# Kernel optimization log

Hardware: AMD Instinct MI355X
Metric: run time of the kernel (lower is better)

The kernel has to match this reference:

```python
import jax, jax.numpy as jnp
import numpy as np

N, E, D, C, L, G = 50000, 1600000, 128, 10, 4, 512
BN_EPS = 1e-5


def setup_inputs() -> dict:
    key = jax.random.key(0)
    ks = jax.random.split(key, 16)
    s = 0.05  # weight init scale
    inp = {
        "x": jax.random.normal(ks[0], (N, D), dtype=jnp.float32),
        "edge_index": jax.random.randint(ks[1], (2, E), 0, N, dtype=jnp.int32),
        "batch": jnp.sort(jax.random.randint(ks[2], (N,), 0, G, dtype=jnp.int32)),
        "num_graphs": G,
        # GINConv inner MLP params (layer 0 input dim == D since num_features == num_hidden)
        "conv_W1": jax.random.normal(ks[3], (L, D, D), dtype=jnp.float32) * s,
        "conv_b1": jnp.zeros((L, D), dtype=jnp.float32),
        "conv_bn_g": jnp.ones((L, D), dtype=jnp.float32),
        "conv_bn_b": jnp.zeros((L, D), dtype=jnp.float32),
        "conv_W2": jax.random.normal(ks[4], (L, D, D), dtype=jnp.float32) * s,
        "conv_b2": jnp.zeros((L, D), dtype=jnp.float32),
        # outer BatchNorm after each conv
        "bn_g": jnp.ones((L, D), dtype=jnp.float32),
        "bn_b": jnp.zeros((L, D), dtype=jnp.float32),
        # per-scale classifier heads (L+1 of them; fcs[0] input dim == num_features == D)
        "fc_W": jax.random.normal(ks[5], (L + 1, D, C), dtype=jnp.float32) * s,
        "fc_b": jnp.zeros((L + 1, C), dtype=jnp.float32),
    }
    return inp


def _bn(h, g, b):
    # BatchNorm1d in training mode: batch stats over nodes, biased variance
    m = h.mean(axis=0)
    v = jnp.mean((h - m) ** 2, axis=0)
    return (h - m) * jax.lax.rsqrt(v + BN_EPS) * g + b


def reference(x, edge_index, batch, num_graphs, conv_W1, conv_b1, conv_bn_g,
              conv_bn_b, conv_W2, conv_b2, bn_g, bn_b, fc_W, fc_b):
    n_nodes = x.shape[0]
    src, dst = edge_index[0], edge_index[1]
    outs = [x]
    h = x
    for i in range(L):
        # GINConv (eps=0, aggr='add'): mlp(x + scatter_add of neighbor features)
        agg = jax.ops.segment_sum(h[src], dst, num_segments=n_nodes)  # [N, D]
        z = h + agg
        z = z @ conv_W1[i] + conv_b1[i]
        z = jax.nn.relu(_bn(z, conv_bn_g[i], conv_bn_b[i]))
        z = z @ conv_W2[i] + conv_b2[i]
        h = jax.nn.relu(_bn(z, bn_g[i], bn_b[i]))
        outs.append(h)
    out = None
    for i, o in enumerate(outs):
        pooled = jax.ops.segment_sum(o, batch, num_segments=num_graphs)  # [G, D]
        logits = pooled @ fc_W[i] + fc_b[i]
        out = logits if out is None else out + logits
    return jax.nn.log_softmax(out, axis=-1)
```

## Files before the change

### kernel.cpp

```cpp
#include <hip/hip_runtime.h>

#define NN 50000
#define EE 1600000
#define DD 128
#define CC 10
#define LLAY 4
#define GG 512
#define GD (GG*DD)
#define NB 196
#define BK_EDGES 1600
#define BUCKCAP 16000
#define NSUB 16
#define SUBW 3125
#define WPAD 136

static constexpr float BN_EPS = 1e-5f;
static constexpr float INV_N = 1.0f / (float)NN;

typedef __bf16 bf16x8 __attribute__((ext_vector_type(8)));
typedef float f32x4 __attribute__((ext_vector_type(4)));

static __device__ __forceinline__ float bflo(unsigned u){ return __uint_as_float(u << 16); }
static __device__ __forceinline__ float bfhi(unsigned u){ return __uint_as_float(u & 0xffff0000u); }
static __device__ __forceinline__ unsigned short f2bf(float f){
    unsigned u = __float_as_uint(f);
    return (unsigned short)((u + 0x7fffu + ((u >> 16) & 1u)) >> 16);
}
static __device__ __forceinline__ unsigned packbf(float a, float b){
    return (unsigned)f2bf(a) | ((unsigned)f2bf(b) << 16);
}
static __device__ __forceinline__ bf16x8 ldfrag(const unsigned short* p){
    union { uint4 u; bf16x8 b; } t; t.u = *(const uint4*)p; return t.b;
}
static __device__ __forceinline__ bf16x8 asfrag(uint4 u){
    union { uint4 u; bf16x8 b; } t; t.u = u; return t.b;
}


__global__ void zero_k(int* p, int n){
    int i = blockIdx.x * 256 + threadIdx.x;
    if (i < n) p[i] = 0;
}

__global__ void wprep_k(const float* __restrict__ W1, const float* __restrict__ W2,
                        unsigned short* __restrict__ Wtall){
    int idx = blockIdx.x * 256 + threadIdx.x;
    int mat = idx >> 14; int rr = idx & 16383;
    int k = rr >> 7; int j = rr & 127;
    const float* Wsrc = (mat < 4) ? (W1 + mat * 16384) : (W2 + (mat - 4) * 16384);
    Wtall[mat * 16384 + j * 128 + k] = f2bf(Wsrc[k * 128 + j]);
}

__global__ void gsearch_k(const int* __restrict__ batch, int* __restrict__ gstart){
    int g = blockIdx.x * 256 + threadIdx.x;
    if (g <= GG){
        int lo = 0, hi = NN;
        while (lo < hi){ int mid = (lo + hi) >> 1; if (batch[mid] < g) lo = mid + 1; else hi = mid; }
        gstart[g] = lo;
    }
}

__global__ __launch_bounds__(256) void binA_k(const int* __restrict__ srcA,
                                              const int* __restrict__ dstA,
                                              int* __restrict__ bucketCur,
                                              unsigned* __restrict__ binned){
    __shared__ int cnt[NB], bas[NB], off[NB];
    int tid = threadIdx.x;
    if (tid < NB){ cnt[tid] = 0; off[tid] = 0; }
    __syncthreads();
    int e0 = blockIdx.x * BK_EDGES;
    for (int i = tid; i < BK_EDGES; i += 256){
        int e = e0 + i;
        if (e < EE) atomicAdd(&cnt[dstA[e] >> 8], 1);
    }
    __syncthreads();
    if (tid < NB && cnt[tid] > 0) bas[tid] = atomicAdd(&bucketCur[tid], cnt[tid]);
    __syncthreads();
    for (int i = tid; i < BK_EDGES; i += 256){
        int e = e0 + i;
        if (e < EE){
            int d = dstA[e]; int b = d >> 8;
            int p = b * BUCKCAP + bas[b] + atomicAdd(&off[b], 1);
            binned[p] = (unsigned)srcA[e] | ((unsigned)(d & 255) << 17);
        }
    }
}

__global__ __launch_bounds__(256) void bscan_k(const int* __restrict__ bucketCur,
                                               int* __restrict__ bucketBase,
                                               int* __restrict__ rp){
    __shared__ int lds[256];
    int t = threadIdx.x;
    int v = (t < NB) ? bucketCur[t] : 0;
    lds[t] = v; __syncthreads();
    for (int o = 1; o < 256; o <<= 1){
        int xv = 0; if (t >= o) xv = lds[t - o];
        __syncthreads(); lds[t] += xv; __syncthreads();
    }
    int excl = lds[t] - v;
    if (t < NB) bucketBase[t] = excl;
    if (t == 0){ bucketBase[NB] = EE; rp[NN] = EE; }
}

__global__ __launch_bounds__(1024) void binB_k(const unsigned* __restrict__ binned,
                                               const int* __restrict__ bucketCur,
                                               const int* __restrict__ bucketBase,
                                               int* __restrict__ rp,
                                               int* __restrict__ ssort){
    __shared__ int c16[256 * NSUB];
    __shared__ int b16[256 * NSUB];
    __shared__ int nt[256];
    int b = blockIdx.x, tid = threadIdx.x;
    int nb0 = b * 256;
    int nmax = NN - nb0; if (nmax > 256) nmax = 256;
    for (int i = tid; i < 256 * NSUB; i += 1024) c16[i] = 0;
    __syncthreads();
    int cntb = bucketCur[b];
    int src0 = b * BUCKCAP;
    int base = bucketBase[b];
    for (int i = tid; i < cntb; i += 1024){
        unsigned u = binned[src0 + i];
        int src = (int)(u & 0x1FFFFu); int dl = (int)(u >> 17);
        atomicAdd(&c16[dl * NSUB + src / SUBW], 1);
    }
    __syncthreads();
    int cc[NSUB]; int tot = 0;
    if (tid < 256){
        #pragma unroll
        for (int k = 0; k < NSUB; k++){ cc[k] = c16[tid * NSUB + k]; tot += cc[k]; }
        nt[tid] = tot;
    }
    __syncthreads();
    for (int o = 1; o < 256; o <<= 1){
        int xv = 0;
        if (tid < 256 && tid >= o) xv = nt[tid - o];
        __syncthreads();
        if (tid < 256) nt[tid] += xv;
        __syncthreads();
    }
    if (tid < 256){
        int p = base + nt[tid] - tot;
        if (tid < nmax) rp[nb0 + tid] = p;
        int run = p;
        #pragma unroll
        for (int k = 0; k < NSUB; k++){ b16[tid * NSUB + k] = run; run += cc[k]; }
    }
    __syncthreads();
    for (int i = tid; i < 256 * NSUB; i += 1024) c16[i] = 0;
    __syncthreads();
    for (int i = tid; i < cntb; i += 1024){
        unsigned u = binned[src0 + i];
        int src = (int)(u & 0x1FFFFu); int dl = (int)(u >> 17);
        int t = src / SUBW;
        int pos = b16[dl * NSUB + t] + atomicAdd(&c16[dl * NSUB + t], 1);
        ssort[pos] = src;
    }
}

__global__ __launch_bounds__(256) void convxpool_k(const float2* __restrict__ x2,
                                                   const int* __restrict__ gstart,
                                                   unsigned* __restrict__ h32,
                                                   float* __restrict__ outp){
    __shared__ float sd[512];
    int b = blockIdx.x; int gid = b >> 2, chunk = b & 3;
    int tid = threadIdx.x; int c = tid & 63, rs = tid >> 6;
    int s = gstart[gid], e = gstart[gid + 1];
    float a0 = 0.f, a1 = 0.f;
    for (int n = s + chunk * 4 + rs; n < e; n += 16){
        float2 v = x2[n * 64 + c];
        h32[n * 64 + c] = packbf(v.x, v.y);
        a0 += v.x; a1 += v.y;
    }
    sd[tid] = a0; sd[256 + tid] = a1; __syncthreads();
    if (tid < 64){
        float r0 = 0.f, r1 = 0.f;
        #pragma unroll
        for (int k2 = 0; k2 < 4; k2++){ r0 += sd[tid + 64 * k2]; r1 += sd[256 + tid + 64 * k2]; }
        atomicAdd(&outp[gid * 128 + 2 * tid], r0);
        atomicAdd(&outp[gid * 128 + 2 * tid + 1], r1);
    }
}


__global__ __launch_bounds__(256) void agg_k(const unsigned* __restrict__ h32,
                                             const int* __restrict__ rp,
                                             const int* __restrict__ ssort,
                                             unsigned* __restrict__ z32,
                                             float* __restrict__ zstats){
    int tid = threadIdx.x;
    if (blockIdx.x == 0) zstats[tid] = 0.f;
    int n = blockIdx.x * 4 + (tid >> 6);
    int lane = tid & 63;
    unsigned self = h32[n * 64 + lane];
    float ax = bflo(self), ay = bfhi(self);
    int e  = __builtin_amdgcn_readfirstlane(rp[n]);
    int e1 = __builtin_amdgcn_readfirstlane(rp[n + 1]);
    for (; e + 15 < e1; e += 16){
        int sA[16];
        #pragma unroll
        for (int k = 0; k < 16; k++) sA[k] = ssort[e + k];
        unsigned uA[16];
        #pragma unroll
        for (int k = 0; k < 16; k++) uA[k] = h32[sA[k] * 64 + lane];
        #pragma unroll
        for (int k = 0; k < 16; k++){ ax += bflo(uA[k]); ay += bfhi(uA[k]); }
    }
    for (; e + 3 < e1; e += 4){
        int s0 = ssort[e], s1 = ssort[e + 1], s2 = ssort[e + 2], s3 = ssort[e + 3];
        unsigned u0 = h32[s0 * 64 + lane];
        unsigned u1 = h32[s1 * 64 + lane];
        unsigned u2 = h32[s2 * 64 + lane];
        unsigned u3 = h32[s3 * 64 + lane];
        ax += bflo(u0) + bflo(u1); ay += bfhi(u0) + bfhi(u1);
        ax += bflo(u2) + bflo(u3); ay += bfhi(u2) + bfhi(u3);
    }
    for (; e < e1; ++e){
        unsigned u0 = h32[ssort[e] * 64 + lane];
        ax += bflo(u0); ay += bfhi(u0);
    }
    z32[n * 64 + lane] = packbf(ax, ay);
}

template<int TR>
__global__ __launch_bounds__(256) void gemm_k(const unsigned* __restrict__ A32,
                                              const unsigned short* __restrict__ Wtg,
                                              const float* __restrict__ bias,
                                              unsigned short* __restrict__ Cst,
                                              const float* __restrict__ stats,
                                              const float* __restrict__ gma,
                                              const float* __restrict__ bta,
                                              float* __restrict__ ostats,
                                              float* __restrict__ zstats,
                                              float* __restrict__ zpool){
    __shared__ __align__(16) unsigned short Wl[64 * WPAD];
    __shared__ float sred[512];
    __shared__ __align__(16) float sl[128], tl[128];
    int tid = threadIdx.x;
    int slice = blockIdx.x & 1;
    int tileb = blockIdx.x >> 1;

    int wv = tid >> 6, lane = tid & 63;
    int rowbase = tileb * 128 + wv * 32;
    int r0 = rowbase + (lane & 15);
    int r1 = r0 + 16;
    int kd = (lane >> 4) * 4;
    uint4 va[4], vb[4];
    #pragma unroll
    for (int ks = 0; ks < 4; ks++){
        va[ks] = (r0 < NN) ? *(const uint4*)(A32 + r0 * 64 + ks * 16 + kd) : make_uint4(0,0,0,0);
        vb[ks] = (r1 < NN) ? *(const uint4*)(A32 + r1 * 64 + ks * 16 + kd) : make_uint4(0,0,0,0);
    }

    if (blockIdx.x == 0 && zstats) zstats[tid] = 0.f;
    if (zpool && blockIdx.x < 256) zpool[blockIdx.x * 256 + tid] = 0.f;
    {
        const uint4* src = (const uint4*)(Wtg + slice * 64 * 128);
        uint4* dst = (uint4*)Wl;
        #pragma unroll
        for (int i = 0; i < 4; i++){
            int idx = tid + 256 * i;
            int row = idx >> 4, c16 = idx & 15;
            dst[row * (WPAD / 8) + c16] = src[idx];
        }
    }
    if (TR && tid < 128){
        float mean = stats[tid] * INV_N;
        float q    = stats[128 + tid] * INV_N;
        float inv  = rsqrtf(q - mean * mean + BN_EPS);
        float s    = gma[tid] * inv;
        sl[tid] = s; tl[tid] = bta[tid] - mean * s;
    }
    __syncthreads();

    if (TR){
        #pragma unroll
        for (int ks = 0; ks < 4; ks++){
            int q = ks * 8 + (lane >> 4) * 2;
            float4 sA = ((const float4*)sl)[q], sB = ((const float4*)sl)[q + 1];
            float4 tA = ((const float4*)tl)[q], tB = ((const float4*)tl)[q + 1];
            float fs[8] = {sA.x, sA.y, sA.z, sA.w, sB.x, sB.y, sB.z, sB.w};
            float ft[8] = {tA.x, tA.y, tA.z, tA.w, tB.x, tB.y, tB.z, tB.w};
            unsigned* pa = (unsigned*)&va[ks];
            unsigned* pb = (unsigned*)&vb[ks];
            #pragma unroll
            for (int c = 0; c < 4; c++){
                float f0 = fmaxf(bflo(pa[c]) * fs[2*c] + ft[2*c], 0.f);
                float f1 = fmaxf(bfhi(pa[c]) * fs[2*c+1] + ft[2*c+1], 0.f);
                pa[c] = packbf(f0, f1);
                f0 = fmaxf(bflo(pb[c]) * fs[2*c] + ft[2*c], 0.f);
                f1 = fmaxf(bfhi(pb[c]) * fs[2*c+1] + ft[2*c+1], 0.f);
                pb[c] = packbf(f0, f1);
            }
        }
    }

    f32x4 acc[2][4];
    #pragma unroll
    for (int a = 0; a < 2; a++)
        #pragma unroll
        for (int b = 0; b < 4; b++) acc[a][b] = (f32x4){0.f, 0.f, 0.f, 0.f};

    #pragma unroll
    for (int ks = 0; ks < 4; ks++){
        int wk = ks * 32 + (lane >> 4) * 8;
        bf16x8 a0 = asfrag(va[ks]);
        bf16x8 a1 = asfrag(vb[ks]);
        #pragma unroll
        for (int ct = 0; ct < 4; ++ct){
            bf16x8 b = ldfrag(&Wl[(ct * 16 + (lane & 15)) * WPAD + wk]);
            acc[0][ct] = __builtin_amdgcn_mfma_f32_16x16x32_bf16(a0, b, acc[0][ct], 0, 0, 0);
            acc[1][ct] = __builtin_amdgcn_mfma_f32_16x16x32_bf16(a1, b, acc[1][ct], 0, 0, 0);
        }
    }

    int cl = lane & 15, rq = lane >> 4;
    float colS[4], colQ[4];
    #pragma unroll
    for (int ct = 0; ct < 4; ++ct){
        int col = slice * 64 + ct * 16 + cl;
        float bv = bias[col];
        float ps = 0.f, pq = 0.f;
        #pragma unroll
        for (int rt = 0; rt < 2; ++rt){
            #pragma unroll
            for (int rr2 = 0; rr2 < 4; ++rr2){
                int grow = rowbase + rt * 16 + rq * 4 + rr2;
                if (grow < NN){
                    float val = acc[rt][ct][rr2] + bv;
                    Cst[grow * 128 + col] = f2bf(val);
                    ps += val; pq += val * val;
                }
            }
        }
        ps += __shfl_xor(ps, 16); pq += __shfl_xor(pq, 16);
        ps += __shfl_xor(ps, 32); pq += __shfl_xor(pq, 32);
        colS[ct] = ps; colQ[ct] = pq;
    }
    if (rq == 0){
        #pragma unroll
        for (int ct = 0; ct < 4; ++ct){
            sred[wv * 64 + ct * 16 + cl]       = colS[ct];
            sred[256 + wv * 64 + ct * 16 + cl] = colQ[ct];
        }
    }
    __syncthreads();
    if (tid < 64){
        float s1 = sred[tid] + sred[64 + tid] + sred[128 + tid] + sred[192 + tid];
        float s2 = sred[256 + tid] + sred[320 + tid] + sred[384 + tid] + sred[448 + tid];
        atomicAdd(&ostats[slice * 64 + tid], s1);
        atomicAdd(&ostats[128 + slice * 64 + tid], s2);
    }
}

__global__ __launch_bounds__(256) void ewpool_k(const unsigned* __restrict__ z32,
                                                const float* __restrict__ stats,
                                                const float* __restrict__ g,
                                                const float* __restrict__ b,
                                                const int* __restrict__ gstart,
                                                unsigned* __restrict__ h32,
                                                float* __restrict__ outp){
    __shared__ float sd[512];
    int blk = blockIdx.x; int gid = blk >> 2, chunk = blk & 3;
    int tid = threadIdx.x;
    int c = tid & 63, rs = tid >> 6;
    int c2 = c * 2;
    float m0 = stats[c2] * INV_N,     q0 = stats[128 + c2] * INV_N;
    float inv0 = rsqrtf(q0 - m0 * m0 + BN_EPS);
    float s0 = g[c2] * inv0, t0 = b[c2] - m0 * s0;
    float m1 = stats[c2 + 1] * INV_N, q1 = stats[129 + c2] * INV_N;
    float inv1 = rsqrtf(q1 - m1 * m1 + BN_EPS);
    float s1 = g[c2 + 1] * inv1, t1 = b[c2 + 1] - m1 * s1;
    int s = gstart[gid], e = gstart[gid + 1];
    float a0 = 0.f, a1 = 0.f;
    int n = s + chunk * 4 + rs;
    for (; n + 16 < e; n += 32){
        unsigned u0 = z32[n * 64 + c];
        unsigned u1 = z32[(n + 16) * 64 + c];
        float f0, f1;
        f0 = fmaxf(bflo(u0) * s0 + t0, 0.f); f1 = fmaxf(bfhi(u0) * s1 + t1, 0.f);
        h32[n * 64 + c] = packbf(f0, f1); a0 += f0; a1 += f1;
        f0 = fmaxf(bflo(u1) * s0 + t0, 0.f); f1 = fmaxf(bfhi(u1) * s1 + t1, 0.f);
        h32[(n + 16) * 64 + c] = packbf(f0, f1); a0 += f0; a1 += f1;
    }
    for (; n < e; n += 16){
        unsigned u = z32[n * 64 + c];
        float f0 = fmaxf(bflo(u) * s0 + t0, 0.f);
        float f1 = fmaxf(bfhi(u) * s1 + t1, 0.f);
        h32[n * 64 + c] = packbf(f0, f1);
        a0 += f0; a1 += f1;
    }
    sd[tid] = a0; sd[256 + tid] = a1; __syncthreads();
    if (tid < 64){
        float r0 = 0.f, r1 = 0.f;
        #pragma unroll
        for (int k2 = 0; k2 < 4; k2++){ r0 += sd[tid + 64 * k2]; r1 += sd[256 + tid + 64 * k2]; }
        atomicAdd(&outp[gid * 128 + 2 * tid], r0);
        atomicAdd(&outp[gid * 128 + 2 * tid + 1], r1);
    }
}

__global__ __launch_bounds__(64) void final_k(const float* __restrict__ pooled,
                                              const float* __restrict__ fcW,
                                              const float* __restrict__ fcb,
                                              float* __restrict__ out){
    int g = blockIdx.x, l = threadIdx.x;
    float p0[5], p1[5];
    #pragma unroll
    for (int i = 0; i < 5; i++){
        p0[i] = pooled[i * GD + g * 128 + l];
        p1[i] = pooled[i * GD + g * 128 + 64 + l];
    }
    float lg[10];
    #pragma unroll
    for (int c2 = 0; c2 < 10; c2++){
        float s = 0;
        #pragma unroll
        for (int i = 0; i < 5; i++){
            s += p0[i] * fcW[(i * 128 + l) * 10 + c2];
            s += p1[i] * fcW[(i * 128 + 64 + l) * 10 + c2];
        }
        #pragma unroll
        for (int off = 32; off >= 1; off >>= 1) s += __shfl_down(s, off);
        lg[c2] = s;
    }
    if (l == 0){
        #pragma unroll
        for (int c2 = 0; c2 < 10; c2++){
            float bs = 0;
            #pragma unroll
            for (int i = 0; i < 5; i++) bs += fcb[i * 10 + c2];
            lg[c2] += bs;
        }
        float mx = lg[0];
        #pragma unroll
        for (int c2 = 1; c2 < 10; c2++) mx = fmaxf(mx, lg[c2]);
        float se = 0;
        #pragma unroll
        for (int c2 = 0; c2 < 10; c2++) se += expf(lg[c2] - mx);
        float lse = mx + logf(se);
        #pragma unroll
        for (int c2 = 0; c2 < 10; c2++) out[g * 10 + c2] = lg[c2] - lse;
    }
}


extern "C" void kernel_launch(void* const* d_in, const int* in_sizes, int n_in,
                              void* d_out, int out_size, void* d_ws, size_t ws_size,
                              hipStream_t stream){
    (void)in_sizes; (void)n_in; (void)out_size; (void)ws_size;
    const float* x     = (const float*)d_in[0];
    const int*   ei    = (const int*)d_in[1];
    const int*   batch = (const int*)d_in[2];
    const float* cW1   = (const float*)d_in[4];
    const float* cb1   = (const float*)d_in[5];
    const float* cbng  = (const float*)d_in[6];
    const float* cbnb  = (const float*)d_in[7];
    const float* cW2   = (const float*)d_in[8];
    const float* cb2   = (const float*)d_in[9];
    const float* bng   = (const float*)d_in[10];
    const float* bnb   = (const float*)d_in[11];
    const float* fcW   = (const float*)d_in[12];
    const float* fcb   = (const float*)d_in[13];

    char* base = (char*)d_ws;
    size_t off = 0;
    auto alloc = [&](size_t bytes) -> void* {
        void* p = base + off;
        off = (off + bytes + 255) & ~(size_t)255;
        return p;
    };
    unsigned*       hB     = (unsigned*)alloc((size_t)NN * 64 * 4);
    unsigned*       zA     = (unsigned*)alloc((size_t)NN * 64 * 4);
    unsigned*       zB     = (unsigned*)alloc((size_t)NN * 64 * 4);
    unsigned short* Wtall  = (unsigned short*)alloc(8 * 16384 * 2);
    int*            ssort  = (int*)alloc((size_t)EE * 4);
    int*            rp     = (int*)alloc((NN + 1) * 4);
    int*            gstart = (int*)alloc((GG + 1) * 4);
    int*            bucketBase = (int*)alloc((NB + 1) * 4);
    int*            bucketCur  = (int*)alloc(NB * 4);
    float*          pooled = (float*)alloc((size_t)5 * GD * 4);
    float*          stats1 = (float*)alloc(256 * 4);
    float*          stats2 = (float*)alloc(256 * 4);
    unsigned*       binned = (unsigned*)zB;

    int zwords = (int)(((char*)(pooled + GD) - (char*)bucketCur) / 4);

    zero_k<<<(zwords + 255) / 256, 256, 0, stream>>>(bucketCur, zwords);
    wprep_k<<<512, 256, 0, stream>>>(cW1, cW2, Wtall);
    gsearch_k<<<3, 256, 0, stream>>>(batch, gstart);
    binA_k<<<(EE + BK_EDGES - 1) / BK_EDGES, 256, 0, stream>>>(ei, ei + EE, bucketCur, binned);
    bscan_k<<<1, 256, 0, stream>>>(bucketCur, bucketBase, rp);
    binB_k<<<NB, 1024, 0, stream>>>(binned, bucketCur, bucketBase, rp, ssort);
    convxpool_k<<<4 * GG, 256, 0, stream>>>((const float2*)x, gstart, hB, pooled);

    const int gemmGrid = 2 * ((NN + 127) / 128);
    for (int i = 0; i < LLAY; i++){
        agg_k<<<NN / 4, 256, 0, stream>>>(hB, rp, ssort, zA, stats1);
        gemm_k<0><<<gemmGrid, 256, 0, stream>>>(zA, Wtall + i * 16384, cb1 + i * 128,
                                                (unsigned short*)zB,
                                                nullptr, nullptr, nullptr, stats1, stats2, nullptr);
        gemm_k<1><<<gemmGrid, 256, 0, stream>>>(zB, Wtall + (4 + i) * 16384, cb2 + i * 128,
                                                (unsigned short*)zA,
                                                stats1, cbng + i * 128, cbnb + i * 128, stats2, nullptr,
                                                pooled + (size_t)(i + 1) * GD);
        ewpool_k<<<4 * GG, 256, 0, stream>>>(zA, stats2, bng + i * 128, bnb + i * 128,
                                             gstart, hB, pooled + (size_t)(i + 1) * GD);
    }
    final_k<<<GG, 64, 0, stream>>>(pooled, fcW, fcb, (float*)d_out);
}
```

Before: 544.7 us.

## Quantize node features to 8-bit for neighbor aggregation gather

Adds per-column max tracking: a max-abs pass over x, and running min/max of the second GEMM output fed through the BN affine. With these, features are stored as 8-bit codes alongside bf16. The aggregation kernel now gathers 1-byte-per-feature rows and sums them with packed integer adds in 16-bit lanes, splitting the wave into two halves that take alternate edge groups. It then dequantizes once per node using the scale and offset times degree. This cuts gather traffic in the memory-bound aggregation, at the cost of 8-bit quantization error in the summed neighbor features, extra kernels and atomics, and a risk of packed-lane overflow at high degree (safe only for degree up to about 257).

```diff
diff --git a/kernel.cpp b/kernel.cpp
--- a/kernel.cpp
+++ b/kernel.cpp
@@ -29,6 +29,14 @@
 static __device__ __forceinline__ unsigned packbf(float a, float b){
     return (unsigned)f2bf(a) | ((unsigned)f2bf(b) << 16);
 }
+static __device__ __forceinline__ unsigned encf(float f){
+    unsigned b = __float_as_uint(f);
+    return (b & 0x80000000u) ? ~b : (b | 0x80000000u);
+}
+static __device__ __forceinline__ float decf(unsigned e){
+    unsigned b = (e & 0x80000000u) ? (e ^ 0x80000000u) : ~e;
+    return __uint_as_float(b);
+}
 static __device__ __forceinline__ bf16x8 ldfrag(const unsigned short* p){
     union { uint4 u; bf16x8 b; } t; t.u = *(const uint4*)p; return t.b;
 }
@@ -157,18 +165,47 @@
     }
 }
 
+__global__ __launch_bounds__(256) void xmax_k(const float* __restrict__ x,
+                                              unsigned* __restrict__ xmaxE){
+    __shared__ float sm[256];
+    int tid = threadIdx.x;
+    int col = tid & 127, rh = tid >> 7;
+    float m = 0.f;
+    for (int r = blockIdx.x * 2 + rh; r < NN; r += 1024)
+        m = fmaxf(m, fabsf(x[r * 128 + col]));
+    sm[tid] = m; __syncthreads();
+    if (tid < 128){
+        m = fmaxf(sm[tid], sm[tid + 128]);
+        atomicMax(&xmaxE[col], __float_as_uint(m));
+    }
+}
+
+__global__ void qx_k(const unsigned* __restrict__ xmaxE,
+                     float* __restrict__ qD, float* __restrict__ qR){
+    int c = threadIdx.x;
+    float m = __uint_as_float(xmaxE[c]);
+    qD[c] = m * (1.f / 127.f);
+    qR[c] = (m > 0.f) ? 127.f / m : 0.f;
+}
+
 __global__ __launch_bounds__(256) void convxpool_k(const float2* __restrict__ x2,
                                                    const int* __restrict__ gstart,
                                                    unsigned* __restrict__ h32,
+                                                   unsigned short* __restrict__ h8u,
+                                                   const float* __restrict__ qR0,
                                                    float* __restrict__ outp){
     __shared__ float sd[512];
     int b = blockIdx.x; int gid = b >> 2, chunk = b & 3;
     int tid = threadIdx.x; int c = tid & 63, rs = tid >> 6;
     int s = gstart[gid], e = gstart[gid + 1];
+    float2 rv = ((const float2*)qR0)[c];
     float a0 = 0.f, a1 = 0.f;
     for (int n = s + chunk * 4 + rs; n < e; n += 16){
         float2 v = x2[n * 64 + c];
         h32[n * 64 + c] = packbf(v.x, v.y);
+        int i0 = (int)rintf(v.x * rv.x) + 128; i0 = min(max(i0, 0), 255);
+        int i1 = (int)rintf(v.y * rv.y) + 128; i1 = min(max(i1, 0), 255);
+        h8u[n * 64 + c] = (unsigned short)(i0 | (i1 << 8));
         a0 += v.x; a1 += v.y;
     }
     sd[tid] = a0; sd[256 + tid] = a1; __syncthreads();
@@ -183,42 +220,66 @@
 
 
 __global__ __launch_bounds__(256) void agg_k(const unsigned* __restrict__ h32,
+                                             const unsigned char* __restrict__ h8,
                                              const int* __restrict__ rp,
                                              const int* __restrict__ ssort,
+                                             const float* __restrict__ qD,
+                                             float offv,
                                              unsigned* __restrict__ z32,
                                              float* __restrict__ zstats){
     int tid = threadIdx.x;
     if (blockIdx.x == 0) zstats[tid] = 0.f;
     int n = blockIdx.x * 4 + (tid >> 6);
     int lane = tid & 63;
-    unsigned self = h32[n * 64 + lane];
-    float ax = bflo(self), ay = bfhi(self);
+    int grp = lane >> 5;
+    int d   = lane & 31;
+    const unsigned* hq = (const unsigned*)h8;
+    const unsigned M = 0x00FF00FFu;
     int e  = __builtin_amdgcn_readfirstlane(rp[n]);
     int e1 = __builtin_amdgcn_readfirstlane(rp[n + 1]);
-    for (; e + 15 < e1; e += 16){
+    int deg = e1 - e;
+    unsigned accE = 0, accO = 0;
+    for (; e + 31 < e1; e += 32){
         int sA[16];
         #pragma unroll
-        for (int k = 0; k < 16; k++) sA[k] = ssort[e + k];
+        for (int k = 0; k < 16; k++) sA[k] = ssort[e + grp * 16 + k];
         unsigned uA[16];
         #pragma unroll
-        for (int k = 0; k < 16; k++) uA[k] = h32[sA[k] * 64 + lane];
-        #pragma unroll
-        for (int k = 0; k < 16; k++){ ax += bflo(uA[k]); ay += bfhi(uA[k]); }
-    }
-    for (; e + 3 < e1; e += 4){
-        int s0 = ssort[e], s1 = ssort[e + 1], s2 = ssort[e + 2], s3 = ssort[e + 3];
-        unsigned u0 = h32[s0 * 64 + lane];
-        unsigned u1 = h32[s1 * 64 + lane];
-        unsigned u2 = h32[s2 * 64 + lane];
-        unsigned u3 = h32[s3 * 64 + lane];
-        ax += bflo(u0) + bflo(u1); ay += bfhi(u0) + bfhi(u1);
-        ax += bflo(u2) + bflo(u3); ay += bfhi(u2) + bfhi(u3);
-    }
-    for (; e < e1; ++e){
-        unsigned u0 = h32[ssort[e] * 64 + lane];
-        ax += bflo(u0); ay += bfhi(u0);
-    }
-    z32[n * 64 + lane] = packbf(ax, ay);
+        for (int k = 0; k < 16; k++) uA[k] = hq[sA[k] * 32 + d];
+        #pragma unroll
+        for (int k = 0; k < 16; k++){ accE += uA[k] & M; accO += (uA[k] >> 8) & M; }
+    }
+    for (; e + 7 < e1; e += 8){
+        int sA[4];
+        #pragma unroll
+        for (int k = 0; k < 4; k++) sA[k] = ssort[e + grp * 4 + k];
+        #pragma unroll
+        for (int k = 0; k < 4; k++){
+            unsigned u = hq[sA[k] * 32 + d];
+            accE += u & M; accO += (u >> 8) & M;
+        }
+    }
+    for (; e + 1 < e1; e += 2){
+        unsigned u = hq[ssort[e + grp] * 32 + d];
+        accE += u & M; accO += (u >> 8) & M;
+    }
+    if (e < e1 && grp == 0){
+        unsigned u = hq[ssort[e] * 32 + d];
+        accE += u & M; accO += (u >> 8) & M;
+    }
+    accE += __shfl_xor(accE, 32);
+    accO += __shfl_xor(accO, 32);
+    if (grp == 0){
+        float4 qd = ((const float4*)qD)[d];
+        uint2 sv = ((const uint2*)(h32 + (size_t)n * 64))[d];
+        float degoff = offv * (float)deg;
+        float z0 = bflo(sv.x) + qd.x * ((float)(accE & 0xFFFFu) - degoff);
+        float z1 = bfhi(sv.x) + qd.y * ((float)(accO & 0xFFFFu) - degoff);
+        float z2 = bflo(sv.y) + qd.z * ((float)(accE >> 16)     - degoff);
+        float z3 = bfhi(sv.y) + qd.w * ((float)(accO >> 16)     - degoff);
+        uint2 o; o.x = packbf(z0, z1); o.y = packbf(z2, z3);
+        ((uint2*)(z32 + (size_t)n * 64))[d] = o;
+    }
 }
 
 template<int TR>
@@ -231,9 +292,10 @@
                                               const float* __restrict__ bta,
                                               float* __restrict__ ostats,
                                               float* __restrict__ zstats,
-                                              float* __restrict__ zpool){
+                                              float* __restrict__ zpool,
+                                              unsigned* __restrict__ mst){
     __shared__ __align__(16) unsigned short Wl[64 * WPAD];
-    __shared__ float sred[512];
+    __shared__ float sred[1024];
     __shared__ __align__(16) float sl[128], tl[128];
     int tid = threadIdx.x;
     int slice = blockIdx.x & 1;
@@ -320,6 +382,7 @@
         int col = slice * 64 + ct * 16 + cl;
         float bv = bias[col];
         float ps = 0.f, pq = 0.f;
+        float vx = -3.4e38f, vn = -3.4e38f;
         #pragma unroll
         for (int rt = 0; rt < 2; ++rt){
             #pragma unroll
@@ -329,12 +392,21 @@
                     float val = acc[rt][ct][rr2] + bv;
                     Cst[grow * 128 + col] = f2bf(val);
                     ps += val; pq += val * val;
+                    if (TR){ vx = fmaxf(vx, val); vn = fmaxf(vn, -val); }
                 }
             }
         }
         ps += __shfl_xor(ps, 16); pq += __shfl_xor(pq, 16);
         ps += __shfl_xor(ps, 32); pq += __shfl_xor(pq, 32);
         colS[ct] = ps; colQ[ct] = pq;
+        if (TR){
+            vx = fmaxf(vx, __shfl_xor(vx, 16)); vx = fmaxf(vx, __shfl_xor(vx, 32));
+            vn = fmaxf(vn, __shfl_xor(vn, 16)); vn = fmaxf(vn, __shfl_xor(vn, 32));
+            if (rq == 0){
+                sred[512 + wv * 64 + ct * 16 + cl] = vx;
+                sred[768 + wv * 64 + ct * 16 + cl] = vn;
+            }
+        }
     }
     if (rq == 0){
         #pragma unroll
@@ -349,6 +421,14 @@
         float s2 = sred[256 + tid] + sred[320 + tid] + sred[384 + tid] + sred[448 + tid];
         atomicAdd(&ostats[slice * 64 + tid], s1);
         atomicAdd(&ostats[128 + slice * 64 + tid], s2);
+        if (TR){
+            float mx = fmaxf(fmaxf(sred[512 + tid], sred[576 + tid]),
+                             fmaxf(sred[640 + tid], sred[704 + tid]));
+            float mn = fmaxf(fmaxf(sred[768 + tid], sred[832 + tid]),
+                             fmaxf(sred[896 + tid], sred[960 + tid]));
+            atomicMax(&mst[slice * 64 + tid], encf(mx));
+            atomicMax(&mst[128 + slice * 64 + tid], encf(mn));
+        }
     }
 }
 
@@ -358,6 +438,9 @@
                                                 const float* __restrict__ b,
                                                 const int* __restrict__ gstart,
                                                 unsigned* __restrict__ h32,
+                                                unsigned short* __restrict__ h8u,
+                                                const unsigned* __restrict__ mst,
+                                                float* __restrict__ qDn,
                                                 float* __restrict__ outp){
     __shared__ float sd[512];
     int blk = blockIdx.x; int gid = blk >> 2, chunk = blk & 3;
@@ -370,23 +453,27 @@
     float m1 = stats[c2 + 1] * INV_N, q1 = stats[129 + c2] * INV_N;
     float inv1 = rsqrtf(q1 - m1 * m1 + BN_EPS);
     float s1 = g[c2 + 1] * inv1, t1 = b[c2 + 1] - m1 * s1;
+    float zx0 = decf(mst[c2]),      zn0 = -decf(mst[128 + c2]);
+    float zx1 = decf(mst[c2 + 1]),  zn1 = -decf(mst[129 + c2]);
+    float hm0 = fmaxf(fmaxf(s0 * zx0 + t0, s0 * zn0 + t0), 0.f);
+    float hm1 = fmaxf(fmaxf(s1 * zx1 + t1, s1 * zn1 + t1), 0.f);
+    float r80 = (hm0 > 0.f) ? 255.f / hm0 : 0.f;
+    float r81 = (hm1 > 0.f) ? 255.f / hm1 : 0.f;
+    if (blk == 0 && rs == 0){
+        qDn[c2]     = hm0 * (1.f / 255.f);
+        qDn[c2 + 1] = hm1 * (1.f / 255.f);
+    }
     int s = gstart[gid], e = gstart[gid + 1];
     float a0 = 0.f, a1 = 0.f;
     int n = s + chunk * 4 + rs;
-    for (; n + 16 < e; n += 32){
-        unsigned u0 = z32[n * 64 + c];
-        unsigned u1 = z32[(n + 16) * 64 + c];
-        float f0, f1;
-        f0 = fmaxf(bflo(u0) * s0 + t0, 0.f); f1 = fmaxf(bfhi(u0) * s1 + t1, 0.f);
-        h32[n * 64 + c] = packbf(f0, f1); a0 += f0; a1 += f1;
-        f0 = fmaxf(bflo(u1) * s0 + t0, 0.f); f1 = fmaxf(bfhi(u1) * s1 + t1, 0.f);
-        h32[(n + 16) * 64 + c] = packbf(f0, f1); a0 += f0; a1 += f1;
-    }
     for (; n < e; n += 16){
         unsigned u = z32[n * 64 + c];
         float f0 = fmaxf(bflo(u) * s0 + t0, 0.f);
         float f1 = fmaxf(bfhi(u) * s1 + t1, 0.f);
         h32[n * 64 + c] = packbf(f0, f1);
+        unsigned cu0 = (unsigned)(f0 * r80 + 0.5f); if (cu0 > 255u) cu0 = 255u;
+        unsigned cu1 = (unsigned)(f1 * r81 + 0.5f); if (cu1 > 255u) cu1 = 255u;
+        h8u[n * 64 + c] = (unsigned short)(cu0 | (cu1 << 8));
         a0 += f0; a1 += f1;
     }
     sd[tid] = a0; sd[256 + tid] = a1; __syncthreads();
@@ -472,15 +559,20 @@
     unsigned*       hB     = (unsigned*)alloc((size_t)NN * 64 * 4);
     unsigned*       zA     = (unsigned*)alloc((size_t)NN * 64 * 4);
     unsigned*       zB     = (unsigned*)alloc((size_t)NN * 64 * 4);
+    unsigned short* h8     = (unsigned short*)alloc((size_t)NN * 64 * 2);
     unsigned short* Wtall  = (unsigned short*)alloc(8 * 16384 * 2);
     int*            ssort  = (int*)alloc((size_t)EE * 4);
     int*            rp     = (int*)alloc((NN + 1) * 4);
     int*            gstart = (int*)alloc((GG + 1) * 4);
     int*            bucketBase = (int*)alloc((NB + 1) * 4);
     int*            bucketCur  = (int*)alloc(NB * 4);
+    unsigned*       xmaxE  = (unsigned*)alloc(128 * 4);
+    unsigned*       mstats = (unsigned*)alloc((size_t)LLAY * 256 * 4);
     float*          pooled = (float*)alloc((size_t)5 * GD * 4);
     float*          stats1 = (float*)alloc(256 * 4);
     float*          stats2 = (float*)alloc(256 * 4);
+    float*          qD     = (float*)alloc(5 * 128 * 4);
+    float*          qR     = (float*)alloc(128 * 4);
     unsigned*       binned = (unsigned*)zB;
 
     int zwords = (int)(((char*)(pooled + GD) - (char*)bucketCur) / 4);
@@ -491,20 +583,27 @@
     binA_k<<<(EE + BK_EDGES - 1) / BK_EDGES, 256, 0, stream>>>(ei, ei + EE, bucketCur, binned);
     bscan_k<<<1, 256, 0, stream>>>(bucketCur, bucketBase, rp);
     binB_k<<<NB, 1024, 0, stream>>>(binned, bucketCur, bucketBase, rp, ssort);
-    convxpool_k<<<4 * GG, 256, 0, stream>>>((const float2*)x, gstart, hB, pooled);
+    xmax_k<<<512, 256, 0, stream>>>(x, xmaxE);
+    qx_k<<<1, 128, 0, stream>>>(xmaxE, qD, qR);
+    convxpool_k<<<4 * GG, 256, 0, stream>>>((const float2*)x, gstart, hB, h8, qR, pooled);
 
     const int gemmGrid = 2 * ((NN + 127) / 128);
     for (int i = 0; i < LLAY; i++){
-        agg_k<<<NN / 4, 256, 0, stream>>>(hB, rp, ssort, zA, stats1);
+        agg_k<<<NN / 4, 256, 0, stream>>>(hB, (const unsigned char*)h8, rp, ssort,
+                                          qD + i * 128, (i == 0) ? 128.f : 0.f, zA, stats1);
         gemm_k<0><<<gemmGrid, 256, 0, stream>>>(zA, Wtall + i * 16384, cb1 + i * 128,
                                                 (unsigned short*)zB,
-                                                nullptr, nullptr, nullptr, stats1, stats2, nullptr);
+                                                nullptr, nullptr, nullptr, stats1, stats2,
+                                                nullptr, nullptr);
         gemm_k<1><<<gemmGrid, 256, 0, stream>>>(zB, Wtall + (4 + i) * 16384, cb2 + i * 128,
                                                 (unsigned short*)zA,
-                                                stats1, cbng + i * 128, cbnb + i * 128, stats2, nullptr,
-                                                pooled + (size_t)(i + 1) * GD);
+                                                stats1, cbng + i * 128, cbnb + i * 128, stats2,
+                                                nullptr, pooled + (size_t)(i + 1) * GD,
+                                                mstats + (size_t)i * 256);
         ewpool_k<<<4 * GG, 256, 0, stream>>>(zA, stats2, bng + i * 128, bnb + i * 128,
-                                             gstart, hB, pooled + (size_t)(i + 1) * GD);
+                                             gstart, hB, h8, mstats + (size_t)i * 256,
+                                             qD + (i + 1) * 128,
+                                             pooled + (size_t)(i + 1) * GD);
     }
     final_k<<<GG, 64, 0, stream>>>(pooled, fcW, fcb, (float*)d_out);
 }
```

Result: slower. 555.9 us (+2.0%).
